# Kernel optimization log

Hardware: AMD Instinct MI355X
Metric: run time of the kernel (lower is better)

## Reference

```python
import jax, jax.numpy as jnp
import numpy as np
from math import sqrt

D_MODEL = 1024
B, T = 4, 4096


def setup_inputs() -> dict:
    key = jax.random.key(0)
    kx, kqk, kvo = jax.random.split(key, 3)
    x = jax.random.normal(kx, (B, T, D_MODEL), dtype=jnp.float32)
    # xavier_uniform for square [D, D]: limit = sqrt(6 / (D + D))
    limit = sqrt(6.0 / (2 * D_MODEL))
    QK = jax.random.uniform(kqk, (D_MODEL, D_MODEL), minval=-limit, maxval=limit, dtype=jnp.float32)
    VO = jax.random.uniform(kvo, (D_MODEL, D_MODEL), minval=-limit, maxval=limit, dtype=jnp.float32)
    return {"x": x, "QK": QK, "VO": VO}


def reference(x, QK, VO):
    d_model = QK.shape[0]
    # scores[b,t,u] = x[b,t,:] @ QK @ x[b,u,:]  -- precompute xQK once
    xQK = jnp.einsum('btd,de->bte', x, QK)                 # [B,T,D]
    scores = jnp.einsum('bte,bue->btu', xQK, x) / sqrt(d_model)  # [B,T,T]
    attn = jax.nn.softmax(scores, axis=2)
    # out[b,t,e] = attn @ x @ VO
    av = jnp.einsum('btu,bud->btd', attn, x)               # [B,T,D]
    return jnp.einsum('btd,de->bte', av, VO)
```

## Files before the change

kernel.cpp:

```cpp
#include <hip/hip_runtime.h>
#include <hip/hip_bf16.h>


#define BB 4
#define TT 4096
#define DD 1024

typedef __attribute__((ext_vector_type(8))) short bf16x8;
typedef __attribute__((ext_vector_type(4))) float f32x4;

__device__ __forceinline__ void gll16(const void* g, void* l) {
  __builtin_amdgcn_global_load_lds(
      (__attribute__((address_space(1))) void*)g,
      (__attribute__((address_space(3))) void*)l, 16, 0, 0);
}

#define WAIT_VM(n) asm volatile("s_waitcnt vmcnt(" #n ")" ::: "memory")
#define WAIT_LGKM0 do { asm volatile("s_waitcnt lgkmcnt(0)" ::: "memory"); \
                        __builtin_amdgcn_sched_barrier(0); } while (0)
#define BARRIER    __builtin_amdgcn_s_barrier()

__global__ __launch_bounds__(256) void xprep_k(const float* __restrict__ in,
                                               __hip_bfloat16* __restrict__ rm,
                                               __hip_bfloat16* __restrict__ cm,
                                               int R, int C, long bs) {
  in += (long)blockIdx.z * bs; rm += (long)blockIdx.z * bs; cm += (long)blockIdx.z * bs;
  __shared__ __hip_bfloat16 tile[64][65];
  int c0 = blockIdx.x * 64, r0 = blockIdx.y * 64;
  int tx = threadIdx.x & 63, ty = threadIdx.x >> 6;
#pragma unroll
  for (int i = 0; i < 16; ++i) {
    int r = ty + i * 4;
    __hip_bfloat16 v = __float2bfloat16(in[(long)(r0 + r) * C + c0 + tx]);
    tile[r][tx] = v;
    rm[(long)(r0 + r) * C + c0 + tx] = v;
  }
  __syncthreads();
#pragma unroll
  for (int i = 0; i < 16; ++i) {
    int c = ty + i * 4;
    cm[(long)(c0 + c) * R + r0 + tx] = tile[tx][c];
  }
}

__global__ __launch_bounds__(256) void transpose_cast_k(const float* __restrict__ in,
                                                        __hip_bfloat16* __restrict__ out,
                                                        int R, int C) {
  __shared__ __hip_bfloat16 tile[64][65];
  int c0 = blockIdx.x * 64, r0 = blockIdx.y * 64;
  int tx = threadIdx.x & 63, ty = threadIdx.x >> 6;
#pragma unroll
  for (int i = 0; i < 16; ++i) {
    int r = ty + i * 4;
    tile[r][tx] = __float2bfloat16(in[(long)(r0 + r) * C + c0 + tx]);
  }
  __syncthreads();
#pragma unroll
  for (int i = 0; i < 16; ++i) {
    int c = ty + i * 4;
    out[(long)(c0 + c) * R + r0 + tx] = tile[tx][c];
  }
}

__global__ __launch_bounds__(256) void zero_f32_k(float* __restrict__ p, int n) {
  int i = blockIdx.x * 256 + threadIdx.x;
  if (i < n) p[i] = 0.f;
}

template <typename OUT_T, int EPI>
__global__ __launch_bounds__(512, 2) void gemm256(
    const __hip_bfloat16* __restrict__ A,
    const __hip_bfloat16* __restrict__ Bt,
    OUT_T* __restrict__ C,
    int M, int N, int K, float alpha,
    long sAz, long sBz, long sCz, float* __restrict__ lsum) {
  __shared__ alignas(16) char smem[131072];
  A  += (long)blockIdx.z * sAz;
  Bt += (long)blockIdx.z * sBz;
  C  += (long)blockIdx.z * sCz;

  const int nwg = gridDim.x * gridDim.y;
  const int lin = blockIdx.x + gridDim.x * blockIdx.y;
  const int swz = (lin & 7) * (nwg >> 3) + (lin >> 3);
  const int gxsh = __popc(gridDim.x - 1);
  const int bx = swz & (gridDim.x - 1);
  const int by = swz >> gxsh;

  const int tid  = threadIdx.x;
  const int lane = tid & 63;
  const int wid  = tid >> 6;
  const int wr   = wid >> 2;
  const int wc   = wid & 3;
  const long m0 = (long)bx * 256;
  const long n0 = (long)by * 256;
  const int NT = K >> 6;

  const int srow = tid >> 3;
  const int sswz = (tid & 7) ^ (srow & 7);
  const __hip_bfloat16* gA = A  + (m0 + srow) * (long)K + sswz * 8;
  const __hip_bfloat16* gB = Bt + (n0 + srow) * (long)K + sswz * 8;

#define STG_A(s, c, D) gll16(gA + (long)(c) * 64 * K + (long)(s) * 64, \
                             smem + (D) + (c) * 8192 + wid * 1024)
#define STG_B(s, c, D) gll16(gB + (long)(c) * 64 * K + (long)(s) * 64, \
                             smem + (D) + 32768 + (c) * 8192 + wid * 1024)

  const int fr = lane & 15, l4 = lane >> 4, f7 = lane & 7;
  const char* a00 = smem +         (wr * 128 + fr) * 128 + ((l4    ) ^ f7) * 16;
  const char* a01 = smem +         (wr * 128 + fr) * 128 + ((4 | l4) ^ f7) * 16;
  const char* b00 = smem + 32768 + (wc * 64  + fr) * 128 + ((l4    ) ^ f7) * 16;
  const char* b01 = smem + 32768 + (wc * 64  + fr) * 128 + ((4 | l4) ^ f7) * 16;
  const char* a10 = a00 + 65536; const char* a11 = a01 + 65536;
  const char* b10 = b00 + 65536; const char* b11 = b01 + 65536;

  bf16x8 aq[4][2], bq[4][2];
#define RD_A(p0, p1, MIOFF)                                         \
  _Pragma("unroll") for (int mi_ = 0; mi_ < 4; ++mi_) {             \
    aq[mi_][0] = *(const bf16x8*)((p0) + ((MIOFF) + mi_) * 2048);   \
    aq[mi_][1] = *(const bf16x8*)((p1) + ((MIOFF) + mi_) * 2048);   \
  }
#define RD_B(p0, p1, NI0)                                           \
  _Pragma("unroll") for (int ni_ = 0; ni_ < 2; ++ni_) {             \
    bq[(NI0) + ni_][0] = *(const bf16x8*)((p0) + ((NI0) + ni_) * 2048); \
    bq[(NI0) + ni_][1] = *(const bf16x8*)((p1) + ((NI0) + ni_) * 2048); \
  }

  f32x4 acc[8][4];
#pragma unroll
  for (int mi = 0; mi < 8; ++mi)
#pragma unroll
    for (int ni = 0; ni < 4; ++ni)
      acc[mi][ni] = (f32x4){0.f, 0.f, 0.f, 0.f};

#define MFMA16(MI0, NI0)                                                       \
  do {                                                                         \
    __builtin_amdgcn_s_setprio(1);                                             \
    _Pragma("unroll") for (int ks_ = 0; ks_ < 2; ++ks_)                        \
    _Pragma("unroll") for (int mi_ = 0; mi_ < 4; ++mi_)                        \
    _Pragma("unroll") for (int ni_ = 0; ni_ < 2; ++ni_)                        \
      acc[(MI0) + mi_][(NI0) + ni_] = __builtin_amdgcn_mfma_f32_16x16x32_bf16( \
          aq[mi_][ks_], bq[(NI0) + ni_][ks_], acc[(MI0) + mi_][(NI0) + ni_],   \
          0, 0, 0);                                                            \
    __builtin_amdgcn_s_setprio(0);                                             \
  } while (0)

#pragma unroll
  for (int c = 0; c < 4; ++c) STG_B(0, c, 0);
#pragma unroll
  for (int c = 0; c < 4; ++c) STG_A(0, c, 0);
#pragma unroll
  for (int c = 0; c < 4; ++c) STG_B(1, c, 65536);
  WAIT_VM(4);
  BARRIER;

  for (int t2 = 0; t2 < NT; t2 += 2) {
    const bool g = (t2 + 2 < NT);
    RD_A(a00, a01, 0); RD_B(b00, b01, 0);
    STG_A(t2 + 1, 0, 65536); STG_A(t2 + 1, 1, 65536);
    asm volatile("s_waitcnt lgkmcnt(8)");
    BARRIER; WAIT_LGKM0; MFMA16(0, 0); BARRIER;
    RD_B(b00, b01, 2);
    STG_A(t2 + 1, 2, 65536); STG_A(t2 + 1, 3, 65536);
    BARRIER; WAIT_LGKM0; MFMA16(0, 2); BARRIER;
    RD_A(a00, a01, 4);
    if (g) { STG_B(t2 + 2, 0, 0); STG_B(t2 + 2, 1, 0); }
    BARRIER; WAIT_LGKM0; MFMA16(4, 2); BARRIER;
    if (g) { STG_B(t2 + 2, 2, 0); STG_B(t2 + 2, 3, 0); }
    MFMA16(4, 0);
    if (g) { WAIT_VM(4); } else { WAIT_VM(0); }
    BARRIER;
    RD_A(a10, a11, 0); RD_B(b10, b11, 0);
    if (g) { STG_A(t2 + 2, 0, 0); STG_A(t2 + 2, 1, 0); }
    asm volatile("s_waitcnt lgkmcnt(8)");
    BARRIER; WAIT_LGKM0; MFMA16(0, 0); BARRIER;
    RD_B(b10, b11, 2);
    if (g) { STG_A(t2 + 2, 2, 0); STG_A(t2 + 2, 3, 0); }
    BARRIER; WAIT_LGKM0; MFMA16(0, 2); BARRIER;
    RD_A(a10, a11, 4);
    if (g) { STG_B(t2 + 3, 0, 65536); STG_B(t2 + 3, 1, 65536); }
    BARRIER; WAIT_LGKM0; MFMA16(4, 2); BARRIER;
    if (g) { STG_B(t2 + 3, 2, 65536); STG_B(t2 + 3, 3, 65536); }
    MFMA16(4, 0);
    if (g) { WAIT_VM(4); }
    BARRIER;
  }

  if constexpr (EPI == 2) {
    float* lred = (float*)smem;
    __syncthreads();
    for (int i = tid; i < 1024; i += 512) lred[i] = 0.f;
    __syncthreads();
#pragma unroll
    for (int mi = 0; mi < 8; ++mi) {
#pragma unroll
      for (int r = 0; r < 4; ++r) {
        const int rloc = wr * 128 + mi * 16 + (l4 << 2) + r;
        const long row = m0 + rloc;
        float rs = 0.f;
#pragma unroll
        for (int ni = 0; ni < 4; ++ni) {
          float e = __expf(acc[mi][ni][r] * alpha);
          long col = n0 + wc * 64 + ni * 16 + fr;
          C[row * (long)N + col] = (OUT_T)__float2bfloat16(e);
          rs += e;
        }
        rs += __shfl_xor(rs, 1); rs += __shfl_xor(rs, 2);
        rs += __shfl_xor(rs, 4); rs += __shfl_xor(rs, 8);
        if (fr == 0) lred[rloc * 4 + wc] = rs;
      }
    }
    __syncthreads();
    if (tid < 256) {
      float s4 = lred[tid * 4] + lred[tid * 4 + 1] + lred[tid * 4 + 2] + lred[tid * 4 + 3];
      atomicAdd(&lsum[(long)blockIdx.z * M + m0 + tid], s4);
    }
  } else if constexpr (EPI == 3) {
#pragma unroll
    for (int mi = 0; mi < 8; ++mi) {
      const long row = m0 + wr * 128 + mi * 16 + (l4 << 2);
      float4 lv = *(const float4*)&lsum[(long)blockIdx.z * M + row];
      float inv[4] = {1.f / lv.x, 1.f / lv.y, 1.f / lv.z, 1.f / lv.w};
#pragma unroll
      for (int ni = 0; ni < 4; ++ni) {
        long col = n0 + wc * 64 + ni * 16 + fr;
#pragma unroll
        for (int r = 0; r < 4; ++r)
          C[(row + r) * (long)N + col] = (OUT_T)__float2bfloat16(acc[mi][ni][r] * inv[r]);
      }
    }
  } else {
#pragma unroll
    for (int mi = 0; mi < 8; ++mi)
#pragma unroll
      for (int ni = 0; ni < 4; ++ni)
#pragma unroll
        for (int r = 0; r < 4; ++r) {
          long row = m0 + wr * 128 + mi * 16 + (l4 << 2) + r;
          long col = n0 + wc * 64 + ni * 16 + fr;
          float v = acc[mi][ni][r] * alpha;
          if constexpr (EPI == 0)
            C[row * (long)N + col] = v;
          else
            C[row * (long)N + col] = (OUT_T)__float2bfloat16(v);
        }
  }
#undef STG_A
#undef STG_B
#undef RD_A
#undef RD_B
#undef MFMA16
}

extern "C" void kernel_launch(void* const* d_in, const int* in_sizes, int n_in,
                              void* d_out, int out_size, void* d_ws, size_t ws_size,
                              hipStream_t stream) {
  const float* x  = (const float*)d_in[0];
  const float* QK = (const float*)d_in[1];
  const float* VO = (const float*)d_in[2];
  char* ws = (char*)d_ws;

  const long MB = 1l << 20;
  __hip_bfloat16* QKT  = (__hip_bfloat16*)(ws);
  float*          lsum = (float*)(ws);
  __hip_bfloat16* VOT  = (__hip_bfloat16*)(ws + 2 * MB);
  __hip_bfloat16* xb   = (__hip_bfloat16*)(ws + 4 * MB);
  __hip_bfloat16* xT   = (__hip_bfloat16*)(ws + 36 * MB);
  __hip_bfloat16* attn = (__hip_bfloat16*)(ws + 68 * MB);
  __hip_bfloat16* xqk  = (__hip_bfloat16*)d_out;

  const long NTOK = (long)BB * TT;
  const long bstride = (long)TT * DD;
  const long aslot = (long)TT * TT;

  xprep_k<<<dim3(DD / 64, TT / 64, BB), 256, 0, stream>>>(x, xb, xT, TT, DD, bstride);
  transpose_cast_k<<<dim3(16, 16, 1), 256, 0, stream>>>(QK, QKT, DD, DD);
  transpose_cast_k<<<dim3(16, 16, 1), 256, 0, stream>>>(VO, VOT, DD, DD);

  gemm256<__hip_bfloat16, 1><<<dim3(TT / 256, DD / 256, BB), 512, 0, stream>>>(
      xb, QKT, xqk, TT, DD, DD, 1.0f, bstride, 0, bstride, nullptr);

  zero_f32_k<<<(int)(NTOK / 256), 256, 0, stream>>>(lsum, (int)NTOK);

  gemm256<__hip_bfloat16, 2><<<dim3(TT / 256, TT / 256, BB), 512, 0, stream>>>(
      xqk, xb, attn, TT, TT, DD, 0.03125f, bstride, bstride, aslot, lsum);

  gemm256<__hip_bfloat16, 3><<<dim3(TT / 256, DD / 256, BB), 512, 0, stream>>>(
      attn, xT, xb, TT, DD, TT, 1.0f, aslot, bstride, bstride, lsum);

  gemm256<float, 0><<<dim3((int)(NTOK / 256), DD / 256, 1), 512, 0, stream>>>(
      xb, VOT, (float*)d_out, (int)NTOK, DD, DD, 1.0f, 0, 0, 0, nullptr);
}
```

Before: 361.3 us.

## Reschedule GEMM prefetch stages and drop per-MFMA-block trailing barriers

Reorders the global-to-LDS prefetch schedule in the main GEMM loop: half of the next B tile is issued earlier and the rest is deferred alongside A loads, with vmcnt waits loosened to 2. It also removes the barrier after each MFMA block, keeping only one barrier per phase. The aim is to cut synchronisation stalls and keep more loads in flight while MFMAs run. The risk is LDS read/write hazards if the reduced barriers and waits no longer protect every buffer reuse.

Result: faster. 345.3 us (-4.4%).

```diff
diff --git a/kernel.cpp b/kernel.cpp
--- a/kernel.cpp
+++ b/kernel.cpp
@@ -145,44 +145,40 @@
   } while (0)
 
 #pragma unroll
+  for (int c = 0; c < 4; ++c) STG_A(0, c, 0);
+#pragma unroll
   for (int c = 0; c < 4; ++c) STG_B(0, c, 0);
-#pragma unroll
-  for (int c = 0; c < 4; ++c) STG_A(0, c, 0);
-#pragma unroll
-  for (int c = 0; c < 4; ++c) STG_B(1, c, 65536);
-  WAIT_VM(4);
+  STG_B(1, 0, 65536); STG_B(1, 1, 65536);
+  WAIT_VM(2);
   BARRIER;
 
   for (int t2 = 0; t2 < NT; t2 += 2) {
     const bool g = (t2 + 2 < NT);
     RD_A(a00, a01, 0); RD_B(b00, b01, 0);
+    STG_B(t2 + 1, 2, 65536); STG_B(t2 + 1, 3, 65536);
     STG_A(t2 + 1, 0, 65536); STG_A(t2 + 1, 1, 65536);
     asm volatile("s_waitcnt lgkmcnt(8)");
-    BARRIER; WAIT_LGKM0; MFMA16(0, 0); BARRIER;
+    BARRIER; WAIT_LGKM0; MFMA16(0, 0);
     RD_B(b00, b01, 2);
     STG_A(t2 + 1, 2, 65536); STG_A(t2 + 1, 3, 65536);
-    BARRIER; WAIT_LGKM0; MFMA16(0, 2); BARRIER;
+    BARRIER; WAIT_LGKM0; MFMA16(0, 2);
     RD_A(a00, a01, 4);
-    if (g) { STG_B(t2 + 2, 0, 0); STG_B(t2 + 2, 1, 0); }
-    BARRIER; WAIT_LGKM0; MFMA16(4, 2); BARRIER;
-    if (g) { STG_B(t2 + 2, 2, 0); STG_B(t2 + 2, 3, 0); }
-    MFMA16(4, 0);
-    if (g) { WAIT_VM(4); } else { WAIT_VM(0); }
-    BARRIER;
+    BARRIER; WAIT_LGKM0; MFMA16(4, 2);
+    if (g) { STG_B(t2 + 2, 0, 0); STG_B(t2 + 2, 1, 0); WAIT_VM(2); }
+    else   { WAIT_VM(0); }
+    BARRIER; MFMA16(4, 0);
     RD_A(a10, a11, 0); RD_B(b10, b11, 0);
-    if (g) { STG_A(t2 + 2, 0, 0); STG_A(t2 + 2, 1, 0); }
+    if (g) { STG_B(t2 + 2, 2, 0); STG_B(t2 + 2, 3, 0);
+             STG_A(t2 + 2, 0, 0); STG_A(t2 + 2, 1, 0); }
     asm volatile("s_waitcnt lgkmcnt(8)");
-    BARRIER; WAIT_LGKM0; MFMA16(0, 0); BARRIER;
+    BARRIER; WAIT_LGKM0; MFMA16(0, 0);
     RD_B(b10, b11, 2);
     if (g) { STG_A(t2 + 2, 2, 0); STG_A(t2 + 2, 3, 0); }
-    BARRIER; WAIT_LGKM0; MFMA16(0, 2); BARRIER;
+    BARRIER; WAIT_LGKM0; MFMA16(0, 2);
     RD_A(a10, a11, 4);
-    if (g) { STG_B(t2 + 3, 0, 65536); STG_B(t2 + 3, 1, 65536); }
-    BARRIER; WAIT_LGKM0; MFMA16(4, 2); BARRIER;
-    if (g) { STG_B(t2 + 3, 2, 65536); STG_B(t2 + 3, 3, 65536); }
-    MFMA16(4, 0);
-    if (g) { WAIT_VM(4); }
-    BARRIER;
+    BARRIER; WAIT_LGKM0; MFMA16(4, 2);
+    if (g) { STG_B(t2 + 3, 0, 65536); STG_B(t2 + 3, 1, 65536); WAIT_VM(2); }
+    BARRIER; MFMA16(4, 0);
   }
 
   if constexpr (EPI == 2) {
```
